# Optimization experiments

Hardware: AMD Instinct MI355X
Metric: run time of the kernel (lower is better)

## Reference

```python
import jax, jax.numpy as jnp
import numpy as np

N_NODES = 100000   # B*A = 4 * 25000 nodes after the reshape in forward()
N_EDGES = 1600000  # avg degree 16
F_IN = 2           # node_features
HID = 64           # hidden_size
K = 3              # diffusion order (hardcoded in RecurrentGCN)


def _glorot(key, shape):
    fan_in, fan_out = shape[-2], shape[-1]
    s = float(np.sqrt(6.0 / (fan_in + fan_out)))
    return jax.random.uniform(key, shape, jnp.float32, -s, s)


def setup_inputs() -> dict:
    key = jax.random.key(0)
    ks = jax.random.split(key, 12)
    x = jax.random.normal(ks[0], (4, 25000, 12, F_IN), dtype=jnp.float32)
    edge_index = jax.random.randint(ks[1], (2, N_EDGES), 0, N_NODES, dtype=jnp.int32)
    edge_weight = jax.random.uniform(ks[2], (N_EDGES,), dtype=jnp.float32)

    def cell(k, cin):
        kw = jax.random.split(k, 3)
        # 3 gates (z, r, h), each a DConv with weight [2, K, cin, HID]
        W = jnp.stack([_glorot(kw[i], (2, K, cin, HID)) for i in range(3)])
        b = jnp.zeros((3, HID), dtype=jnp.float32)
        return W, b

    enc1_W, enc1_b = cell(ks[3], F_IN + HID)
    enc2_W, enc2_b = cell(ks[4], HID + HID)
    dec1_W, dec1_b = cell(ks[5], F_IN + HID)
    dec2_W, dec2_b = cell(ks[6], HID + HID)
    lin_W = _glorot(ks[7], (HID, F_IN))
    lin_b = jnp.zeros((F_IN,), dtype=jnp.float32)
    return dict(x=x, edge_index=edge_index, edge_weight=edge_weight,
                enc1_W=enc1_W, enc1_b=enc1_b, enc2_W=enc2_W, enc2_b=enc2_b,
                dec1_W=dec1_W, dec1_b=dec1_b, dec2_W=dec2_W, dec2_b=dec2_b,
                lin_W=lin_W, lin_b=lin_b)


def _dconv(v, src, dst, do_inv, di_inv, W, b):
    # Dual-direction diffusion conv (DConv, torch_geometric_temporal), order K.
    # Normalization is applied at the node level before gather so the
    # edge-level multiply (E x C) never needs to be a stored residual.
    def pout(u):  # out[dst] += deg_out_inv[src] * u[src]
        return jax.ops.segment_sum((do_inv[:, None] * u)[src], dst, num_segments=N_NODES)

    def pin(u):   # out[src] += deg_in_inv[dst] * u[dst]
        return jax.ops.segment_sum((di_inv[:, None] * u)[dst], src, num_segments=N_NODES)

    H = v @ (W[0, 0] + W[1, 0])
    t1o, t1i = pout(v), pin(v)
    H = H + t1o @ W[0, 1] + t1i @ W[1, 1]
    t0o = t0i = v
    for k in range(2, K):  # Chebyshev-style recurrence
        t2o = 2.0 * pout(t1o) - t0o
        t2i = 2.0 * pin(t1i) - t0i
        H = H + t2o @ W[0, k] + t2i @ W[1, k]
        t0o, t1o = t1o, t2o
        t0i, t1i = t1i, t2i
    return H + b


def _dcrnn(x, h, src, dst, do_inv, di_inv, W, b):
    # GRU cell whose gates are diffusion convolutions over [x, h].
    xh = jnp.concatenate([x, h], axis=1)
    Z = jax.nn.sigmoid(_dconv(xh, src, dst, do_inv, di_inv, W[0], b[0]))
    R = jax.nn.sigmoid(_dconv(xh, src, dst, do_inv, di_inv, W[1], b[1]))
    Ht = jnp.tanh(_dconv(jnp.concatenate([x, R * h], axis=1),
                         src, dst, do_inv, di_inv, W[2], b[2]))
    return Z * h + (1.0 - Z) * Ht


def _forward(x, edge_index, edge_weight,
             enc1_W, enc1_b, enc2_W, enc2_b,
             dec1_W, dec1_b, dec2_W, dec2_b, lin_W, lin_b):
    B, A, S, Fd = x.shape
    # permute(0,1,3,2) then [..., 0] == x[:, :, 0, :]; flatten to [B*A, F]
    xs = x[:, :, 0, :].reshape(B * A, Fd)
    src, dst = edge_index[0], edge_index[1]
    deg_out = jax.ops.segment_sum(edge_weight, src, num_segments=N_NODES)
    deg_in = jax.ops.segment_sum(edge_weight, dst, num_segments=N_NODES)
    do_inv = jnp.where(deg_out > 0, 1.0 / deg_out, 0.0)
    di_inv = jnp.where(deg_in > 0, 1.0 / deg_in, 0.0)
    zeros = jnp.zeros((B * A, HID), dtype=x.dtype)
    h_enc1 = _dcrnn(xs, zeros, src, dst, do_inv, di_inv, enc1_W, enc1_b)
    h = jax.nn.relu(h_enc1)
    h_enc2 = _dcrnn(h, zeros, src, dst, do_inv, di_inv, enc2_W, enc2_b)
    h = _dcrnn(xs, h_enc1, src, dst, do_inv, di_inv, dec1_W, dec1_b)
    h = jax.nn.relu(h)
    h = _dcrnn(h, h_enc2, src, dst, do_inv, di_inv, dec2_W, dec2_b)
    return h @ lin_W + lin_b


def reference(x, edge_index, edge_weight,
              enc1_W, enc1_b, enc2_W, enc2_b,
              dec1_W, dec1_b, dec2_W, dec2_b, lin_W, lin_b):
    return _forward(x, edge_index, edge_weight,
                    enc1_W, enc1_b, enc2_W, enc2_b,
                    dec1_W, dec1_b, dec2_W, dec2_b, lin_W, lin_b)
```

## Files before the change

### kernel.cpp

```cpp
#include <hip/hip_runtime.h>

#define N_NODES 100000
#define N_EDGES 1600000

typedef _Float16 f16;
typedef _Float16 f16x4 __attribute__((ext_vector_type(4)));
typedef _Float16 f16x8 __attribute__((ext_vector_type(8)));
typedef float f32x4 __attribute__((ext_vector_type(4)));

__device__ __forceinline__ float sigf(float x) { return 1.f / (1.f + __expf(-x)); }


__global__ void count_kernel(const int* __restrict__ src, const int* __restrict__ dst,
                             int* __restrict__ cntO, int* __restrict__ cntI,
                             int* __restrict__ slotO, int* __restrict__ slotI)
{
    int i = blockIdx.x * 256 + threadIdx.x;
    if (i >= N_EDGES) return;
    slotO[i] = atomicAdd(&cntO[dst[i]], 1);
    slotI[i] = atomicAdd(&cntI[src[i]], 1);
}

__global__ __launch_bounds__(1024) void scan2_kernel(const int* __restrict__ cntA, int* __restrict__ rpA,
                                                     const int* __restrict__ cntB, int* __restrict__ rpB,
                                                     int n)
{
    const int* cnt = blockIdx.x ? cntB : cntA;
    int* rp = blockIdx.x ? rpB : rpA;
    __shared__ int wsum[16];
    __shared__ int carry;
    int tid = threadIdx.x, lane = tid & 63, wid = tid >> 6;
    if (tid == 0) { rp[0] = 0; carry = 0; }
    __syncthreads();
    for (int base = 0; base < n; base += 1024) {
        int idx = base + tid;
        int x = (idx < n) ? cnt[idx] : 0;
        #pragma unroll
        for (int off = 1; off < 64; off <<= 1) {
            int y = __shfl_up(x, off);
            if (lane >= off) x += y;
        }
        if (lane == 63) wsum[wid] = x;
        __syncthreads();
        if (wid == 0 && lane < 16) {
            int y = wsum[lane];
            #pragma unroll
            for (int off = 1; off < 16; off <<= 1) {
                int z = __shfl_up(y, off);
                if (lane >= off) y += z;
            }
            wsum[lane] = y;
        }
        __syncthreads();
        int tot = x + (wid ? wsum[wid - 1] : 0) + carry;
        if (idx < n) rp[idx + 1] = tot;
        __syncthreads();
        if (tid == 1023) carry = tot;
        __syncthreads();
    }
}

__global__ void fill_kernel(const int* __restrict__ src, const int* __restrict__ dst,
                            const float* __restrict__ ew,
                            const int* __restrict__ rpO, const int* __restrict__ rpI,
                            const int* __restrict__ slotO, const int* __restrict__ slotI,
                            int2* __restrict__ adj2O, int2* __restrict__ adj2I)
{
    int i = blockIdx.x * 256 + threadIdx.x;
    if (i >= N_EDGES) return;
    int s = src[i], d = dst[i];
    int wb = __float_as_int(ew[i]);
    int2 eo; eo.x = s; eo.y = wb;
    adj2O[rpO[d] + slotO[i]] = eo;
    int2 ei; ei.x = d; ei.y = wb;
    adj2I[rpI[s] + slotI[i]] = ei;
}

__global__ void finalize_kernel(const int* __restrict__ rpO, const int2* __restrict__ adj2O,
                                int* __restrict__ adjO, float* __restrict__ di_inv,
                                const int* __restrict__ rpI, const int2* __restrict__ adj2I,
                                int* __restrict__ adjI, float* __restrict__ do_inv)
{
    int n = blockIdx.x * 256 + threadIdx.x;
    if (n >= N_NODES) return;
    float s = 0.f;
    for (int e = rpO[n]; e < rpO[n + 1]; ++e) {
        int2 v = adj2O[e];
        adjO[e] = v.x;
        s += __int_as_float(v.y);
    }
    di_inv[n] = (s > 0.f) ? 1.f / s : 0.f;
    float t = 0.f;
    for (int e = rpI[n]; e < rpI[n + 1]; ++e) {
        int2 v = adj2I[e];
        adjI[e] = v.x;
        t += __int_as_float(v.y);
    }
    do_inv[n] = (t > 0.f) ? 1.f / t : 0.f;
}

__global__ void prep_w(const float* __restrict__ W, int C, int rowBase,
                       int gLo, int gHi, int COLS, int XSTEP, f16* __restrict__ outw)
{
    int total = (10 + XSTEP) * COLS * 32;
    int idx = blockIdx.x * 256 + threadIdx.x;
    if (idx >= total) return;
    int k32 = idx & 31;
    int c = (idx >> 5) % COLS;
    int s = (idx >> 5) / COLS;
    int g = (c < 64 || gHi < 0) ? gLo : gHi;
    int col = (c >= 64) ? c - 64 : c;
    int p, r;
    if (s < 10) { p = s >> 1; r = rowBase + ((s & 1) << 5) + k32; }
    else {
        if (k32 < 10) { p = k32 >> 1; r = k32 & 1; }
        else { outw[idx] = (f16)0.f; return; }
    }
    auto wv = [&](int d, int k) {
        return W[((((size_t)(g * 2 + d) * 3 + k) * C + r) << 6) + col];
    };
    float val;
    if (p == 0)      val = wv(0, 0) + wv(1, 0) - wv(0, 2) - wv(1, 2);
    else if (p == 1) val = wv(0, 1);
    else if (p == 2) val = 2.f * wv(0, 2);
    else if (p == 3) val = wv(1, 1);
    else             val = 2.f * wv(1, 2);
    outw[idx] = (f16)val;
}

__global__ void prep_enc1w(const float* __restrict__ W, float* __restrict__ outw)
{
    int idx = blockIdx.x * 256 + threadIdx.x;
    if (idx >= 1280) return;
    int c = idx & 127, k = idx >> 7;
    int g = (c < 64) ? 0 : 2, col = c & 63;
    int p = k >> 1, r = k & 1;
    const int C = 66;
    auto wv = [&](int d, int kk) {
        return W[((((size_t)(g * 2 + d) * 3 + kk) * C + r) << 6) + col];
    };
    float val;
    if (p == 0)      val = wv(0, 0) + wv(1, 0) - wv(0, 2) - wv(1, 2);
    else if (p == 1) val = wv(0, 1);
    else if (p == 2) val = 2.f * wv(0, 2);
    else if (p == 3) val = wv(1, 1);
    else             val = 2.f * wv(1, 2);
    outw[idx] = val;
}

__global__ void xcat_init(const float* __restrict__ x, f16* __restrict__ xcat)
{
    int i = blockIdx.x * 256 + threadIdx.x;
    if (i >= N_NODES * 32) return;
    int n = i >> 5, c = i & 31;
    float v = (c < 2) ? x[(size_t)n * 24 + c] : 0.f;
    xcat[i] = (f16)v;
}

__global__ void prop2_kernel(const int* __restrict__ rp, const int* __restrict__ adj,
                             const float* __restrict__ scale, f16* __restrict__ xcat,
                             int cin, int cout)
{
    int n = blockIdx.x * 256 + threadIdx.x;
    if (n >= N_NODES) return;
    int beg = rp[n], end = rp[n + 1];
    float a0 = 0.f, a1 = 0.f;
    for (int e = beg; e < end; ++e) {
        int s = adj[e];
        float w = scale[s];
        a0 += w * (float)xcat[((size_t)s << 5) + cin];
        a1 += w * (float)xcat[((size_t)s << 5) + cin + 1];
    }
    xcat[((size_t)n << 5) + cout] = (f16)a0;
    xcat[((size_t)n << 5) + cout + 1] = (f16)a1;
}

__global__ __launch_bounds__(256) void prop8(
    const int* __restrict__ rpA, const int* __restrict__ adjA, const float* __restrict__ scA,
    const f16* __restrict__ uA, f16* __restrict__ outA,
    const int* __restrict__ rpB, const int* __restrict__ adjB, const float* __restrict__ scB,
    const f16* __restrict__ uB, f16* __restrict__ outB)
{
    const int* RP; const int* ADJ; const float* SC; const f16* U; f16* OUT;
    if (blockIdx.y == 0) { RP = rpA; ADJ = adjA; SC = scA; U = uA; OUT = outA; }
    else                 { RP = rpB; ADJ = adjB; SC = scB; U = uB; OUT = outB; }
    int tid = threadIdx.x;
    int node = blockIdx.x * 32 + (tid >> 3);
    int l = tid & 7;
    if (node >= N_NODES) return;
    int b = RP[node], e = RP[node + 1];
    float a0 = 0.f, a1 = 0.f, a2 = 0.f, a3 = 0.f;
    float a4 = 0.f, a5 = 0.f, a6 = 0.f, a7 = 0.f;
    float c0 = 0.f, c1 = 0.f, c2 = 0.f, c3 = 0.f;
    float c4 = 0.f, c5 = 0.f, c6 = 0.f, c7 = 0.f;
    int i = b;
    for (; i + 1 < e; i += 2) {
        int s0 = ADJ[i], s1 = ADJ[i + 1];
        float w0 = SC[s0], w1 = SC[s1];
        f16x8 u0 = *(const f16x8*)(U + (((size_t)s0 << 6) + (l << 3)));
        f16x8 u1 = *(const f16x8*)(U + (((size_t)s1 << 6) + (l << 3)));
        a0 += w0 * (float)u0[0]; a1 += w0 * (float)u0[1];
        a2 += w0 * (float)u0[2]; a3 += w0 * (float)u0[3];
        a4 += w0 * (float)u0[4]; a5 += w0 * (float)u0[5];
        a6 += w0 * (float)u0[6]; a7 += w0 * (float)u0[7];
        c0 += w1 * (float)u1[0]; c1 += w1 * (float)u1[1];
        c2 += w1 * (float)u1[2]; c3 += w1 * (float)u1[3];
        c4 += w1 * (float)u1[4]; c5 += w1 * (float)u1[5];
        c6 += w1 * (float)u1[6]; c7 += w1 * (float)u1[7];
    }
    if (i < e) {
        int s = ADJ[i];
        float w = SC[s];
        f16x8 u0 = *(const f16x8*)(U + (((size_t)s << 6) + (l << 3)));
        a0 += w * (float)u0[0]; a1 += w * (float)u0[1];
        a2 += w * (float)u0[2]; a3 += w * (float)u0[3];
        a4 += w * (float)u0[4]; a5 += w * (float)u0[5];
        a6 += w * (float)u0[6]; a7 += w * (float)u0[7];
    }
    f16x8 r;
    r[0] = (f16)(a0 + c0); r[1] = (f16)(a1 + c1);
    r[2] = (f16)(a2 + c2); r[3] = (f16)(a3 + c3);
    r[4] = (f16)(a4 + c4); r[5] = (f16)(a5 + c5);
    r[6] = (f16)(a6 + c6); r[7] = (f16)(a7 + c7);
    *(f16x8*)(OUT + (((size_t)node << 6) + (l << 3))) = r;
}

template <int STEPS, int COLS, int ACT>
__global__ __launch_bounds__(256) void mfma_gemm(
    const f16* __restrict__ p0, const f16* __restrict__ p1, const f16* __restrict__ p2,
    const f16* __restrict__ p3, const f16* __restrict__ p4, const f16* __restrict__ xcat,
    const f16* __restrict__ wstep, const f16* __restrict__ addX,
    const float* __restrict__ biasLo, const float* __restrict__ biasHi,
    f16* __restrict__ out, const f16* __restrict__ hmul, f16* __restrict__ out2,
    const f16* __restrict__ zin)
{
    __shared__ f16 As[64][40];
    __shared__ f16 Ws[COLS][40];
    const int row0 = blockIdx.x * 64;
    const int tid = threadIdx.x;
    const int wave = tid >> 6, lane = tid & 63;
    const int lr = lane & 15, lk = lane >> 4;
    const int ka = lk << 3;

    constexpr int RT = (COLS == 128) ? 4 : 2;
    f32x4 acc[RT][2] = {};

    const f16* parts[5] = { p0, p1, p2, p3, p4 };

    #pragma unroll
    for (int s = 0; s < STEPS; ++s) {
        __syncthreads();
        {
            int r = tid >> 2, seg = tid & 3;
            int grow = row0 + r;
            const f16* srcp = (s < 10)
                ? parts[s >> 1] + (((size_t)grow << 6) + ((s & 1) << 5) + (seg << 3))
                : xcat + (((size_t)grow << 5) + (seg << 3));
            int4 v = (grow < N_NODES) ? *(const int4*)srcp : make_int4(0, 0, 0, 0);
            *(int4*)&As[r][seg << 3] = v;
        }
        {
            for (int q = tid; q < COLS * 4; q += 256) {
                int c = q >> 2, seg = q & 3;
                *(int4*)&Ws[c][seg << 3] =
                    *(const int4*)(wstep + (((size_t)(s * COLS + c) << 5) + (seg << 3)));
            }
        }
        __syncthreads();
        if (COLS == 128) {
            f16x8 b0 = *(const f16x8*)&Ws[wave * 32 + lr][ka];
            f16x8 b1 = *(const f16x8*)&Ws[wave * 32 + 16 + lr][ka];
            #pragma unroll
            for (int rt = 0; rt < RT; ++rt) {
                f16x8 a = *(const f16x8*)&As[rt * 16 + lr][ka];
                acc[rt][0] = __builtin_amdgcn_mfma_f32_16x16x32_f16(a, b0, acc[rt][0], 0, 0, 0);
                acc[rt][1] = __builtin_amdgcn_mfma_f32_16x16x32_f16(a, b1, acc[rt][1], 0, 0, 0);
            }
        } else {
            f16x8 b0 = *(const f16x8*)&Ws[(wave & 1) * 32 + lr][ka];
            f16x8 b1 = *(const f16x8*)&Ws[(wave & 1) * 32 + 16 + lr][ka];
            #pragma unroll
            for (int rt = 0; rt < RT; ++rt) {
                f16x8 a = *(const f16x8*)&As[(wave >> 1) * 32 + rt * 16 + lr][ka];
                acc[rt][0] = __builtin_amdgcn_mfma_f32_16x16x32_f16(a, b0, acc[rt][0], 0, 0, 0);
                acc[rt][1] = __builtin_amdgcn_mfma_f32_16x16x32_f16(a, b1, acc[rt][1], 0, 0, 0);
            }
        }
    }
    if constexpr (ACT == 4) {
        __shared__ float zbuf[64][65];
        float treg[RT][2][4];
        #pragma unroll
        for (int rt = 0; rt < RT; ++rt)
            #pragma unroll
            for (int ct = 0; ct < 2; ++ct) {
                int col = wave * 32 + ct * 16 + lr;
                #pragma unroll
                for (int j = 0; j < 4; ++j) {
                    int r = rt * 16 + lk * 4 + j;
                    float v = acc[rt][ct][j] + ((col < 64) ? biasLo[col] : biasHi[col - 64]);
                    if (col < 64) zbuf[r][col] = sigf(v);
                    else          treg[rt][ct][j] = tanhf(v);
                }
            }
        __syncthreads();
        #pragma unroll
        for (int rt = 0; rt < RT; ++rt)
            #pragma unroll
            for (int ct = 0; ct < 2; ++ct) {
                int col = wave * 32 + ct * 16 + lr;
                if (col < 64) continue;
                #pragma unroll
                for (int j = 0; j < 4; ++j) {
                    int r = rt * 16 + lk * 4 + j;
                    int grow = row0 + r;
                    if (grow >= N_NODES) continue;
                    float h = (1.f - zbuf[r][col - 64]) * treg[rt][ct][j];
                    out[((size_t)grow << 6) + (col - 64)] = (f16)h;
                }
            }
    } else if constexpr (ACT == 5) {
        #pragma unroll
        for (int rt = 0; rt < RT; ++rt)
            #pragma unroll
            for (int ct = 0; ct < 2; ++ct) {
                int col = wave * 32 + ct * 16 + lr;
                #pragma unroll
                for (int j = 0; j < 4; ++j) {
                    int grow = row0 + rt * 16 + lk * 4 + j;
                    if (grow >= N_NODES) continue;
                    float v = acc[rt][ct][j];
                    if (addX) v += (float)addX[((size_t)grow << 7) + col];
                    v += (col < 64) ? biasLo[col] : biasHi[col - 64];
                    float sg = sigf(v);
                    if (col < 64)
                        out[((size_t)grow << 6) + col] = (f16)sg;
                    else
                        out2[((size_t)grow << 6) + (col - 64)] =
                            (f16)(sg * (float)hmul[((size_t)grow << 6) + (col - 64)]);
                }
            }
    } else {
        #pragma unroll
        for (int rt = 0; rt < RT; ++rt) {
            int rbase = (COLS == 128) ? rt * 16 : (wave >> 1) * 32 + rt * 16;
            #pragma unroll
            for (int ct = 0; ct < 2; ++ct) {
                int col = ((COLS == 128) ? wave * 32 : (wave & 1) * 32) + ct * 16 + lr;
                #pragma unroll
                for (int j = 0; j < 4; ++j) {
                    int grow = row0 + rbase + lk * 4 + j;
                    if (grow >= N_NODES) continue;
                    float v = acc[rt][ct][j];
                    if (addX)   v += (float)addX[(size_t)grow * COLS + col];
                    if (biasLo) v += (col < 64) ? biasLo[col] : biasHi[col - 64];
                    if (ACT == 1)      v = sigf(v);
                    else if (ACT == 2) v = tanhf(v);
                    else if (ACT == 6) {
                        float t = tanhf(v);
                        float z = (float)zin[((size_t)grow << 6) + col];
                        float hv = (float)hmul[((size_t)grow << 6) + col];
                        v = fmaxf(z * hv + (1.f - z) * t, 0.f);
                    }
                    out[(size_t)grow * COLS + col] = (f16)v;
                }
            }
        }
    }
}

__global__ __launch_bounds__(256) void enc1_kernel(const f16* __restrict__ xcat,
                                                   const float* __restrict__ We1,
                                                   const float* __restrict__ b,
                                                   f16* __restrict__ h1, f16* __restrict__ h1r)
{
    int node = (blockIdx.x << 2) + (threadIdx.x >> 6);
    int lane = threadIdx.x & 63;
    float az = b[lane], at = b[128 + lane];
    #pragma unroll
    for (int k = 0; k < 10; ++k) {
        float xv = (float)xcat[((size_t)node << 5) + k];
        az += xv * We1[k * 128 + lane];
        at += xv * We1[k * 128 + 64 + lane];
    }
    float z = sigf(az), t = tanhf(at);
    float h = (1.f - z) * t;
    size_t o = ((size_t)node << 6) + lane;
    h1[o] = (f16)h;
    h1r[o] = (f16)fmaxf(h, 0.f);
}


__global__ __launch_bounds__(256) void final_kernel(const f16* __restrict__ zb, const f16* __restrict__ gT,
                                                    const f16* __restrict__ h2,
                                                    const float* __restrict__ lW, const float* __restrict__ lb,
                                                    float* __restrict__ out)
{
    int node = (blockIdx.x << 2) + (threadIdx.x >> 6);
    int lane = threadIdx.x & 63;
    size_t i = ((size_t)node << 6) + lane;
    float z = (float)zb[i];
    float d = z * (float)h2[i] + (1.f - z) * (float)gT[i];
    float s0 = d * lW[lane * 2];
    float s1 = d * lW[lane * 2 + 1];
    #pragma unroll
    for (int off = 32; off > 0; off >>= 1) {
        s0 += __shfl_down(s0, off);
        s1 += __shfl_down(s1, off);
    }
    if (lane == 0) {
        out[node * 2]     = s0 + lb[0];
        out[node * 2 + 1] = s1 + lb[1];
    }
}


extern "C" void kernel_launch(void* const* d_in, const int* in_sizes, int n_in,
                              void* d_out, int out_size, void* d_ws, size_t ws_size,
                              hipStream_t stream)
{
    (void)in_sizes; (void)n_in; (void)out_size;
    const float* x   = (const float*)d_in[0];
    const int*  eidx = (const int*)d_in[1];
    const float* ew  = (const float*)d_in[2];
    const float* e1W = (const float*)d_in[3];
    const float* e1b = (const float*)d_in[4];
    const float* e2W = (const float*)d_in[5];
    const float* e2b = (const float*)d_in[6];
    const float* d1W = (const float*)d_in[7];
    const float* d1b = (const float*)d_in[8];
    const float* d2W = (const float*)d_in[9];
    const float* d2b = (const float*)d_in[10];
    const float* lW  = (const float*)d_in[11];
    const float* lb  = (const float*)d_in[12];
    const int* src = eidx;
    const int* dst = eidx + N_EDGES;
    const int N = N_NODES, E = N_EDGES;

    char* p = (char*)d_ws;
    auto carve = [&](size_t bytes) { char* r = p; p += (bytes + 255) & ~(size_t)255; return r; };
    int*   cntO  = (int*)carve((size_t)2 * N * 4);
    int*   cntI  = cntO + N;
    int*   rpO   = (int*)carve((size_t)(N + 1) * 4);
    int*   rpI   = (int*)carve((size_t)(N + 1) * 4);
    int*   slotO = (int*)carve((size_t)E * 4);
    int*   slotI = (int*)carve((size_t)E * 4);
    int2*  adj2O = (int2*)carve((size_t)E * 8);
    int2*  adj2I = (int2*)carve((size_t)E * 8);
    float* do_inv = (float*)carve((size_t)N * 4);
    float* di_inv = (float*)carve((size_t)N * 4);
    f16*   xcat = (f16*)carve((size_t)N * 32 * 2);
    size_t NH = (size_t)N * 64 * 2;
    f16* h1  = (f16*)carve(NH);
    f16* h1r = (f16*)carve(NH);
    f16* h2  = (f16*)carve(NH);
    f16* g   = (f16*)carve(NH);
    f16* gT  = (f16*)carve(NH);
    f16* t0  = (f16*)carve(NH);
    f16* t1  = (f16*)carve(NH);
    f16* t2  = (f16*)carve(NH);
    f16* t3  = (f16*)carve(NH);
    f16* zb  = (f16*)carve(NH);
    f16* zz128 = (f16*)carve((size_t)N * 128 * 2);
    f16* wE2   = (f16*)carve((size_t)10 * 128 * 32 * 2);
    f16* wD1zr = (f16*)carve((size_t)11 * 128 * 32 * 2);
    f16* wD1c  = (f16*)carve((size_t)11 * 64 * 32 * 2);
    f16* wD2zrA = (f16*)carve((size_t)10 * 128 * 32 * 2);
    f16* wD2zrB = (f16*)carve((size_t)10 * 128 * 32 * 2);
    f16* wD2cA  = (f16*)carve((size_t)10 * 64 * 32 * 2);
    f16* wD2cB  = (f16*)carve((size_t)10 * 64 * 32 * 2);
    float* We1  = (float*)carve((size_t)1280 * 4);

    size_t needed = (size_t)(p - (char*)d_ws);
    if (needed > ws_size) return;

    const int eg = (E + 255) / 256;
    const int ng = (N + 255) / 256;
    const int GB = 25000;

    hipMemsetAsync(cntO, 0, (size_t)2 * N * 4, stream);
    count_kernel<<<eg, 256, 0, stream>>>(src, dst, cntO, cntI, slotO, slotI);
    scan2_kernel<<<2, 1024, 0, stream>>>(cntO, rpO, cntI, rpI, N);
    fill_kernel<<<eg, 256, 0, stream>>>(src, dst, ew, rpO, rpI, slotO, slotI, adj2O, adj2I);
    int* adjO = slotO;
    int* adjI = slotI;
    finalize_kernel<<<ng, 256, 0, stream>>>(rpO, adj2O, adjO, di_inv, rpI, adj2I, adjI, do_inv);

    auto wprep = [&](const float* W, int C, int rowBase, int gLo, int gHi, int COLS, int XS, f16* o) {
        int total = (10 + XS) * COLS * 32;
        prep_w<<<(total + 255) / 256, 256, 0, stream>>>(W, C, rowBase, gLo, gHi, COLS, XS, o);
    };
    wprep(e2W, 128, 0,  0, 2, 128, 0, wE2);
    wprep(d1W, 66,  2,  0, 1, 128, 1, wD1zr);
    wprep(d1W, 66,  2,  2, -1, 64, 1, wD1c);
    wprep(d2W, 128, 0,  0, 1, 128, 0, wD2zrA);
    wprep(d2W, 128, 64, 0, 1, 128, 0, wD2zrB);
    wprep(d2W, 128, 0,  2, -1, 64, 0, wD2cA);
    wprep(d2W, 128, 64, 2, -1, 64, 0, wD2cB);
    prep_enc1w<<<5, 256, 0, stream>>>(e1W, We1);

    xcat_init<<<(N * 32 + 255) / 256, 256, 0, stream>>>(x, xcat);
    prop2_kernel<<<ng, 256, 0, stream>>>(rpO, adjO, do_inv, xcat, 0, 2);
    prop2_kernel<<<ng, 256, 0, stream>>>(rpO, adjO, do_inv, xcat, 2, 4);
    prop2_kernel<<<ng, 256, 0, stream>>>(rpI, adjI, di_inv, xcat, 0, 6);
    prop2_kernel<<<ng, 256, 0, stream>>>(rpI, adjI, di_inv, xcat, 6, 8);

    const dim3 pg((N + 31) / 32, 2);
    auto props = [&](const f16* u) {
        prop8<<<pg, 256, 0, stream>>>(rpO, adjO, do_inv, u, t0,
                                      rpI, adjI, di_inv, u, t2);
        prop8<<<pg, 256, 0, stream>>>(rpO, adjO, do_inv, t0, t1,
                                      rpI, adjI, di_inv, t2, t3);
    };
    const int gg = (N + 63) / 64;

    enc1_kernel<<<GB, 256, 0, stream>>>(xcat, We1, e1b, h1, h1r);
    props(h1r);
    mfma_gemm<10, 128, 4><<<gg, 256, 0, stream>>>(h1r, t0, t1, t2, t3, nullptr, wE2,
                                                  nullptr, e2b, e2b + 128, h2, nullptr, nullptr, nullptr);
    props(h1);
    mfma_gemm<11, 128, 5><<<gg, 256, 0, stream>>>(h1, t0, t1, t2, t3, xcat, wD1zr,
                                                  nullptr, d1b, d1b + 64, zb, h1, g, nullptr);
    props(g);
    mfma_gemm<11, 64, 6><<<gg, 256, 0, stream>>>(g, t0, t1, t2, t3, xcat, wD1c,
                                                 nullptr, d1b + 128, d1b + 128, h1r, h1, nullptr, zb);
    props(h1r);
    mfma_gemm<10, 128, 0><<<gg, 256, 0, stream>>>(h1r, t0, t1, t2, t3, nullptr, wD2zrA,
                                                  nullptr, nullptr, nullptr, zz128, nullptr, nullptr, nullptr);
    mfma_gemm<10, 64, 0><<<gg, 256, 0, stream>>>(h1r, t0, t1, t2, t3, nullptr, wD2cA,
                                                 nullptr, nullptr, nullptr, gT, nullptr, nullptr, nullptr);
    props(h2);
    mfma_gemm<10, 128, 5><<<gg, 256, 0, stream>>>(h2, t0, t1, t2, t3, nullptr, wD2zrB,
                                                  zz128, d2b, d2b + 64, zb, h2, g, nullptr);
    props(g);
    mfma_gemm<10, 64, 2><<<gg, 256, 0, stream>>>(g, t0, t1, t2, t3, nullptr, wD2cB,
                                                 gT, d2b + 128, d2b + 128, gT, nullptr, nullptr, nullptr);
    final_kernel<<<GB, 256, 0, stream>>>(zb, gT, h2, lW, lb, (float*)d_out);
}
```

Baseline: 1.480 ms.

## Pack paired hidden states into 128-wide buffers and share diffusion propagations

Hidden-state pairs that are diffused by the same graph operators (relu(h1)/h1, and h1r/h2 for the second decoder cell) are stored side by side in 128-channel buffers. Each pair is then propagated in one pass with 16 lanes per node, so two props calls become one, and the first decoder gate GEMM reuses the encoder propagation results. The two decoder-2 z/r GEMMs merge into one 20-step GEMM, the zz128 intermediate is dropped, and the four prop2 launches are combined into two using a second grid dimension. The propagation scratch now aliases the edge-build buffers. In exchange, the 128-wide gathers read twice as much data per edge, and the grid sizes assume N divides evenly by 16 and 32.

Measured after the change: 1.470 ms. No clear change (-0.6%).

```diff
diff --git a/kernel.cpp b/kernel.cpp
--- a/kernel.cpp
+++ b/kernel.cpp
@@ -4,7 +4,6 @@
 #define N_EDGES 1600000
 
 typedef _Float16 f16;
-typedef _Float16 f16x4 __attribute__((ext_vector_type(4)));
 typedef _Float16 f16x8 __attribute__((ext_vector_type(8)));
 typedef float f32x4 __attribute__((ext_vector_type(4)));
 
@@ -99,10 +98,10 @@
     do_inv[n] = (t > 0.f) ? 1.f / t : 0.f;
 }
 
-__global__ void prep_w(const float* __restrict__ W, int C, int rowBase,
-                       int gLo, int gHi, int COLS, int XSTEP, f16* __restrict__ outw)
-{
-    int total = (10 + XSTEP) * COLS * 32;
+__global__ void prep_w(const float* __restrict__ W, int C, int SA, int PWA, int rA,
+                       int gLo, int gHi, int COLS, int XS, f16* __restrict__ outw)
+{
+    int total = (SA + XS) * COLS * 32;
     int idx = blockIdx.x * 256 + threadIdx.x;
     if (idx >= total) return;
     int k32 = idx & 31;
@@ -111,7 +110,7 @@
     int g = (c < 64 || gHi < 0) ? gLo : gHi;
     int col = (c >= 64) ? c - 64 : c;
     int p, r;
-    if (s < 10) { p = s >> 1; r = rowBase + ((s & 1) << 5) + k32; }
+    if (s < SA) { p = s / PWA; r = rA + (s % PWA) * 32 + k32; }
     else {
         if (k32 < 10) { p = k32 >> 1; r = k32 & 1; }
         else { outw[idx] = (f16)0.f; return; }
@@ -157,17 +156,22 @@
     xcat[i] = (f16)v;
 }
 
-__global__ void prop2_kernel(const int* __restrict__ rp, const int* __restrict__ adj,
-                             const float* __restrict__ scale, f16* __restrict__ xcat,
-                             int cin, int cout)
-{
+__global__ void prop2d_kernel(const int* __restrict__ rpA, const int* __restrict__ adjA,
+                              const float* __restrict__ scA, int cinA, int coutA,
+                              const int* __restrict__ rpB, const int* __restrict__ adjB,
+                              const float* __restrict__ scB, int cinB, int coutB,
+                              f16* __restrict__ xcat)
+{
+    const int* rp; const int* adj; const float* sc; int cin, cout;
+    if (blockIdx.y == 0) { rp = rpA; adj = adjA; sc = scA; cin = cinA; cout = coutA; }
+    else                 { rp = rpB; adj = adjB; sc = scB; cin = cinB; cout = coutB; }
     int n = blockIdx.x * 256 + threadIdx.x;
     if (n >= N_NODES) return;
     int beg = rp[n], end = rp[n + 1];
     float a0 = 0.f, a1 = 0.f;
     for (int e = beg; e < end; ++e) {
         int s = adj[e];
-        float w = scale[s];
+        float w = sc[s];
         a0 += w * (float)xcat[((size_t)s << 5) + cin];
         a1 += w * (float)xcat[((size_t)s << 5) + cin + 1];
     }
@@ -175,64 +179,57 @@
     xcat[((size_t)n << 5) + cout + 1] = (f16)a1;
 }
 
-__global__ __launch_bounds__(256) void prop8(
+template <int LPN>
+__global__ __launch_bounds__(256) void propk(
     const int* __restrict__ rpA, const int* __restrict__ adjA, const float* __restrict__ scA,
-    const f16* __restrict__ uA, f16* __restrict__ outA,
+    const f16* __restrict__ uA, f16* __restrict__ oA,
     const int* __restrict__ rpB, const int* __restrict__ adjB, const float* __restrict__ scB,
-    const f16* __restrict__ uB, f16* __restrict__ outB)
+    const f16* __restrict__ uB, f16* __restrict__ oB,
+    int ldu, int ldo)
 {
     const int* RP; const int* ADJ; const float* SC; const f16* U; f16* OUT;
-    if (blockIdx.y == 0) { RP = rpA; ADJ = adjA; SC = scA; U = uA; OUT = outA; }
-    else                 { RP = rpB; ADJ = adjB; SC = scB; U = uB; OUT = outB; }
-    int tid = threadIdx.x;
-    int node = blockIdx.x * 32 + (tid >> 3);
-    int l = tid & 7;
+    if (blockIdx.y == 0) { RP = rpA; ADJ = adjA; SC = scA; U = uA; OUT = oA; }
+    else                 { RP = rpB; ADJ = adjB; SC = scB; U = uB; OUT = oB; }
+    constexpr int NPB = 256 / LPN;
+    int node = blockIdx.x * NPB + (threadIdx.x / LPN);
+    int l = threadIdx.x % LPN;
     if (node >= N_NODES) return;
     int b = RP[node], e = RP[node + 1];
-    float a0 = 0.f, a1 = 0.f, a2 = 0.f, a3 = 0.f;
-    float a4 = 0.f, a5 = 0.f, a6 = 0.f, a7 = 0.f;
-    float c0 = 0.f, c1 = 0.f, c2 = 0.f, c3 = 0.f;
-    float c4 = 0.f, c5 = 0.f, c6 = 0.f, c7 = 0.f;
+    float a[8] = {0.f, 0.f, 0.f, 0.f, 0.f, 0.f, 0.f, 0.f};
+    float c[8] = {0.f, 0.f, 0.f, 0.f, 0.f, 0.f, 0.f, 0.f};
     int i = b;
     for (; i + 1 < e; i += 2) {
         int s0 = ADJ[i], s1 = ADJ[i + 1];
         float w0 = SC[s0], w1 = SC[s1];
-        f16x8 u0 = *(const f16x8*)(U + (((size_t)s0 << 6) + (l << 3)));
-        f16x8 u1 = *(const f16x8*)(U + (((size_t)s1 << 6) + (l << 3)));
-        a0 += w0 * (float)u0[0]; a1 += w0 * (float)u0[1];
-        a2 += w0 * (float)u0[2]; a3 += w0 * (float)u0[3];
-        a4 += w0 * (float)u0[4]; a5 += w0 * (float)u0[5];
-        a6 += w0 * (float)u0[6]; a7 += w0 * (float)u0[7];
-        c0 += w1 * (float)u1[0]; c1 += w1 * (float)u1[1];
-        c2 += w1 * (float)u1[2]; c3 += w1 * (float)u1[3];
-        c4 += w1 * (float)u1[4]; c5 += w1 * (float)u1[5];
-        c6 += w1 * (float)u1[6]; c7 += w1 * (float)u1[7];
+        f16x8 u0 = *(const f16x8*)(U + (size_t)s0 * ldu + (l << 3));
+        f16x8 u1 = *(const f16x8*)(U + (size_t)s1 * ldu + (l << 3));
+        #pragma unroll
+        for (int j = 0; j < 8; ++j) { a[j] += w0 * (float)u0[j]; c[j] += w1 * (float)u1[j]; }
     }
     if (i < e) {
         int s = ADJ[i];
         float w = SC[s];
-        f16x8 u0 = *(const f16x8*)(U + (((size_t)s << 6) + (l << 3)));
-        a0 += w * (float)u0[0]; a1 += w * (float)u0[1];
-        a2 += w * (float)u0[2]; a3 += w * (float)u0[3];
-        a4 += w * (float)u0[4]; a5 += w * (float)u0[5];
-        a6 += w * (float)u0[6]; a7 += w * (float)u0[7];
+        f16x8 u0 = *(const f16x8*)(U + (size_t)s * ldu + (l << 3));
+        #pragma unroll
+        for (int j = 0; j < 8; ++j) a[j] += w * (float)u0[j];
     }
     f16x8 r;
-    r[0] = (f16)(a0 + c0); r[1] = (f16)(a1 + c1);
-    r[2] = (f16)(a2 + c2); r[3] = (f16)(a3 + c3);
-    r[4] = (f16)(a4 + c4); r[5] = (f16)(a5 + c5);
-    r[6] = (f16)(a6 + c6); r[7] = (f16)(a7 + c7);
-    *(f16x8*)(OUT + (((size_t)node << 6) + (l << 3))) = r;
-}
-
-template <int STEPS, int COLS, int ACT>
+    #pragma unroll
+    for (int j = 0; j < 8; ++j) r[j] = (f16)(a[j] + c[j]);
+    *(f16x8*)(OUT + (size_t)node * ldo + (l << 3)) = r;
+}
+
+template <int SA, int XS, int COLS, int ACT>
 __global__ __launch_bounds__(256) void mfma_gemm(
-    const f16* __restrict__ p0, const f16* __restrict__ p1, const f16* __restrict__ p2,
-    const f16* __restrict__ p3, const f16* __restrict__ p4, const f16* __restrict__ xcat,
-    const f16* __restrict__ wstep, const f16* __restrict__ addX,
+    const f16* __restrict__ uA, const f16* __restrict__ tA0, const f16* __restrict__ tA1,
+    const f16* __restrict__ tA2, const f16* __restrict__ tA3,
+    int lAu, int cAu, int lAt, int cAt,
+    const f16* __restrict__ xcat, const f16* __restrict__ wstep,
+    const f16* __restrict__ addX,
     const float* __restrict__ biasLo, const float* __restrict__ biasHi,
-    f16* __restrict__ out, const f16* __restrict__ hmul, f16* __restrict__ out2,
-    const f16* __restrict__ zin)
+    f16* __restrict__ out, int os,
+    const f16* __restrict__ hmul, int hs,
+    f16* __restrict__ out2, const f16* __restrict__ zin)
 {
     __shared__ f16 As[64][40];
     __shared__ f16 Ws[COLS][40];
@@ -241,11 +238,11 @@
     const int wave = tid >> 6, lane = tid & 63;
     const int lr = lane & 15, lk = lane >> 4;
     const int ka = lk << 3;
-
     constexpr int RT = (COLS == 128) ? 4 : 2;
+    constexpr int PWA = SA / 5;
+    constexpr int STEPS = SA + XS;
     f32x4 acc[RT][2] = {};
-
-    const f16* parts[5] = { p0, p1, p2, p3, p4 };
+    const f16* tA[4] = { tA0, tA1, tA2, tA3 };
 
     #pragma unroll
     for (int s = 0; s < STEPS; ++s) {
@@ -253,18 +250,23 @@
         {
             int r = tid >> 2, seg = tid & 3;
             int grow = row0 + r;
-            const f16* srcp = (s < 10)
-                ? parts[s >> 1] + (((size_t)grow << 6) + ((s & 1) << 5) + (seg << 3))
-                : xcat + (((size_t)grow << 5) + (seg << 3));
+            const f16* srcp;
+            if (s < SA) {
+                int p = s / PWA, ch = s % PWA;
+                const f16* base = (p == 0) ? uA : tA[p - 1];
+                int ld = (p == 0) ? lAu : lAt;
+                int co = (p == 0) ? cAu : cAt;
+                srcp = base + (size_t)grow * ld + co + ch * 32 + (seg << 3);
+            } else {
+                srcp = xcat + (((size_t)grow) << 5) + (seg << 3);
+            }
             int4 v = (grow < N_NODES) ? *(const int4*)srcp : make_int4(0, 0, 0, 0);
             *(int4*)&As[r][seg << 3] = v;
         }
-        {
-            for (int q = tid; q < COLS * 4; q += 256) {
-                int c = q >> 2, seg = q & 3;
-                *(int4*)&Ws[c][seg << 3] =
-                    *(const int4*)(wstep + (((size_t)(s * COLS + c) << 5) + (seg << 3)));
-            }
+        for (int q = tid; q < COLS * 4; q += 256) {
+            int c = q >> 2, seg = q & 3;
+            *(int4*)&Ws[c][seg << 3] =
+                *(const int4*)(wstep + (((size_t)(s * COLS + c)) << 5) + (seg << 3));
         }
         __syncthreads();
         if (COLS == 128) {
@@ -316,7 +318,7 @@
                     int grow = row0 + r;
                     if (grow >= N_NODES) continue;
                     float h = (1.f - zbuf[r][col - 64]) * treg[rt][ct][j];
-                    out[((size_t)grow << 6) + (col - 64)] = (f16)h;
+                    out[(size_t)grow * os + (col - 64)] = (f16)h;
                 }
             }
     } else if constexpr (ACT == 5) {
@@ -329,15 +331,13 @@
                 for (int j = 0; j < 4; ++j) {
                     int grow = row0 + rt * 16 + lk * 4 + j;
                     if (grow >= N_NODES) continue;
-                    float v = acc[rt][ct][j];
-                    if (addX) v += (float)addX[((size_t)grow << 7) + col];
-                    v += (col < 64) ? biasLo[col] : biasHi[col - 64];
+                    float v = acc[rt][ct][j] + ((col < 64) ? biasLo[col] : biasHi[col - 64]);
                     float sg = sigf(v);
                     if (col < 64)
                         out[((size_t)grow << 6) + col] = (f16)sg;
                     else
                         out2[((size_t)grow << 6) + (col - 64)] =
-                            (f16)(sg * (float)hmul[((size_t)grow << 6) + (col - 64)]);
+                            (f16)(sg * (float)hmul[(size_t)grow * hs + (col - 64)]);
                 }
             }
     } else {
@@ -352,17 +352,16 @@
                     int grow = row0 + rbase + lk * 4 + j;
                     if (grow >= N_NODES) continue;
                     float v = acc[rt][ct][j];
-                    if (addX)   v += (float)addX[(size_t)grow * COLS + col];
+                    if (addX)   v += (float)addX[((size_t)grow << 6) + col];
                     if (biasLo) v += (col < 64) ? biasLo[col] : biasHi[col - 64];
-                    if (ACT == 1)      v = sigf(v);
-                    else if (ACT == 2) v = tanhf(v);
+                    if (ACT == 2) v = tanhf(v);
                     else if (ACT == 6) {
                         float t = tanhf(v);
                         float z = (float)zin[((size_t)grow << 6) + col];
-                        float hv = (float)hmul[((size_t)grow << 6) + col];
+                        float hv = (float)hmul[(size_t)grow * hs + col];
                         v = fmaxf(z * hv + (1.f - z) * t, 0.f);
                     }
-                    out[(size_t)grow * COLS + col] = (f16)v;
+                    out[(size_t)grow * os + col] = (f16)v;
                 }
             }
         }
@@ -372,7 +371,7 @@
 __global__ __launch_bounds__(256) void enc1_kernel(const f16* __restrict__ xcat,
                                                    const float* __restrict__ We1,
                                                    const float* __restrict__ b,
-                                                   f16* __restrict__ h1, f16* __restrict__ h1r)
+                                                   f16* __restrict__ c1)
 {
     int node = (blockIdx.x << 2) + (threadIdx.x >> 6);
     int lane = threadIdx.x & 63;
@@ -385,11 +384,10 @@
     }
     float z = sigf(az), t = tanhf(at);
     float h = (1.f - z) * t;
-    size_t o = ((size_t)node << 6) + lane;
-    h1[o] = (f16)h;
-    h1r[o] = (f16)fmaxf(h, 0.f);
-}
-
+    size_t o = (size_t)node * 128 + lane;
+    c1[o] = (f16)fmaxf(h, 0.f);
+    c1[o + 64] = (f16)h;
+}
 
 __global__ __launch_bounds__(256) void final_kernel(const f16* __restrict__ zb, const f16* __restrict__ gT,
                                                     const f16* __restrict__ h2,
@@ -400,7 +398,7 @@
     int lane = threadIdx.x & 63;
     size_t i = ((size_t)node << 6) + lane;
     float z = (float)zb[i];
-    float d = z * (float)h2[i] + (1.f - z) * (float)gT[i];
+    float d = z * (float)h2[(size_t)node * 128 + lane] + (1.f - z) * (float)gT[i];
     float s0 = d * lW[lane * 2];
     float s1 = d * lW[lane * 2 + 1];
     #pragma unroll
@@ -439,37 +437,36 @@
 
     char* p = (char*)d_ws;
     auto carve = [&](size_t bytes) { char* r = p; p += (bytes + 255) & ~(size_t)255; return r; };
+    size_t NC = (size_t)N * 128 * 2;
+    size_t NH = (size_t)N * 64 * 2;
     int*   cntO  = (int*)carve((size_t)2 * N * 4);
     int*   cntI  = cntO + N;
     int*   rpO   = (int*)carve((size_t)(N + 1) * 4);
     int*   rpI   = (int*)carve((size_t)(N + 1) * 4);
     int*   slotO = (int*)carve((size_t)E * 4);
     int*   slotI = (int*)carve((size_t)E * 4);
-    int2*  adj2O = (int2*)carve((size_t)E * 8);
-    int2*  adj2I = (int2*)carve((size_t)E * 8);
+    char*  uni   = carve((size_t)2 * E * 8);
+    int2*  adj2O = (int2*)uni;
+    int2*  adj2I = (int2*)(uni + (size_t)E * 8);
+    f16*   ct0   = (f16*)uni;
+    f16*   ct1   = (f16*)carve(NC);
+    f16*   ct2   = (f16*)carve(NC);
+    f16*   ct3   = (f16*)carve(NC);
     float* do_inv = (float*)carve((size_t)N * 4);
     float* di_inv = (float*)carve((size_t)N * 4);
     f16*   xcat = (f16*)carve((size_t)N * 32 * 2);
-    size_t NH = (size_t)N * 64 * 2;
-    f16* h1  = (f16*)carve(NH);
-    f16* h1r = (f16*)carve(NH);
-    f16* h2  = (f16*)carve(NH);
-    f16* g   = (f16*)carve(NH);
-    f16* gT  = (f16*)carve(NH);
-    f16* t0  = (f16*)carve(NH);
-    f16* t1  = (f16*)carve(NH);
-    f16* t2  = (f16*)carve(NH);
-    f16* t3  = (f16*)carve(NH);
-    f16* zb  = (f16*)carve(NH);
-    f16* zz128 = (f16*)carve((size_t)N * 128 * 2);
+    f16*   c1   = (f16*)carve(NC);
+    f16*   c2   = (f16*)carve(NC);
+    f16*   g    = (f16*)carve(NH);
+    f16*   gT   = (f16*)carve(NH);
+    f16*   zb   = (f16*)carve(NH);
     f16* wE2   = (f16*)carve((size_t)10 * 128 * 32 * 2);
     f16* wD1zr = (f16*)carve((size_t)11 * 128 * 32 * 2);
     f16* wD1c  = (f16*)carve((size_t)11 * 64 * 32 * 2);
-    f16* wD2zrA = (f16*)carve((size_t)10 * 128 * 32 * 2);
-    f16* wD2zrB = (f16*)carve((size_t)10 * 128 * 32 * 2);
-    f16* wD2cA  = (f16*)carve((size_t)10 * 64 * 32 * 2);
-    f16* wD2cB  = (f16*)carve((size_t)10 * 64 * 32 * 2);
-    float* We1  = (float*)carve((size_t)1280 * 4);
+    f16* wD2zr = (f16*)carve((size_t)20 * 128 * 32 * 2);
+    f16* wD2cA = (f16*)carve((size_t)10 * 64 * 32 * 2);
+    f16* wD2cB = (f16*)carve((size_t)10 * 64 * 32 * 2);
+    float* We1 = (float*)carve((size_t)1280 * 4);
 
     size_t needed = (size_t)(p - (char*)d_ws);
     if (needed > ws_size) return;
@@ -486,54 +483,64 @@
     int* adjI = slotI;
     finalize_kernel<<<ng, 256, 0, stream>>>(rpO, adj2O, adjO, di_inv, rpI, adj2I, adjI, do_inv);
 
-    auto wprep = [&](const float* W, int C, int rowBase, int gLo, int gHi, int COLS, int XS, f16* o) {
-        int total = (10 + XS) * COLS * 32;
-        prep_w<<<(total + 255) / 256, 256, 0, stream>>>(W, C, rowBase, gLo, gHi, COLS, XS, o);
+    auto wprep = [&](const float* W, int C, int SA, int PWA, int rA,
+                     int gLo, int gHi, int COLS, int XS, f16* o) {
+        int total = (SA + XS) * COLS * 32;
+        prep_w<<<(total + 255) / 256, 256, 0, stream>>>(W, C, SA, PWA, rA, gLo, gHi, COLS, XS, o);
     };
-    wprep(e2W, 128, 0,  0, 2, 128, 0, wE2);
-    wprep(d1W, 66,  2,  0, 1, 128, 1, wD1zr);
-    wprep(d1W, 66,  2,  2, -1, 64, 1, wD1c);
-    wprep(d2W, 128, 0,  0, 1, 128, 0, wD2zrA);
-    wprep(d2W, 128, 64, 0, 1, 128, 0, wD2zrB);
-    wprep(d2W, 128, 0,  2, -1, 64, 0, wD2cA);
-    wprep(d2W, 128, 64, 2, -1, 64, 0, wD2cB);
+    wprep(e2W, 128, 10, 2, 0,  0,  2, 128, 0, wE2);
+    wprep(d1W, 66,  10, 2, 2,  0,  1, 128, 1, wD1zr);
+    wprep(d1W, 66,  10, 2, 2,  2, -1,  64, 1, wD1c);
+    wprep(d2W, 128, 20, 4, 0,  0,  1, 128, 0, wD2zr);
+    wprep(d2W, 128, 10, 2, 0,  2, -1,  64, 0, wD2cA);
+    wprep(d2W, 128, 10, 2, 64, 2, -1,  64, 0, wD2cB);
     prep_enc1w<<<5, 256, 0, stream>>>(e1W, We1);
 
     xcat_init<<<(N * 32 + 255) / 256, 256, 0, stream>>>(x, xcat);
-    prop2_kernel<<<ng, 256, 0, stream>>>(rpO, adjO, do_inv, xcat, 0, 2);
-    prop2_kernel<<<ng, 256, 0, stream>>>(rpO, adjO, do_inv, xcat, 2, 4);
-    prop2_kernel<<<ng, 256, 0, stream>>>(rpI, adjI, di_inv, xcat, 0, 6);
-    prop2_kernel<<<ng, 256, 0, stream>>>(rpI, adjI, di_inv, xcat, 6, 8);
-
-    const dim3 pg((N + 31) / 32, 2);
-    auto props = [&](const f16* u) {
-        prop8<<<pg, 256, 0, stream>>>(rpO, adjO, do_inv, u, t0,
-                                      rpI, adjI, di_inv, u, t2);
-        prop8<<<pg, 256, 0, stream>>>(rpO, adjO, do_inv, t0, t1,
-                                      rpI, adjI, di_inv, t2, t3);
+    dim3 ng2(ng, 2);
+    prop2d_kernel<<<ng2, 256, 0, stream>>>(rpO, adjO, do_inv, 0, 2,
+                                           rpI, adjI, di_inv, 0, 6, xcat);
+    prop2d_kernel<<<ng2, 256, 0, stream>>>(rpO, adjO, do_inv, 2, 4,
+                                           rpI, adjI, di_inv, 6, 8, xcat);
+
+    auto props128 = [&](const f16* u) {
+        dim3 pg(N / 16, 2);
+        propk<16><<<pg, 256, 0, stream>>>(rpO, adjO, do_inv, u, ct0,
+                                          rpI, adjI, di_inv, u, ct2, 128, 128);
+        propk<16><<<pg, 256, 0, stream>>>(rpO, adjO, do_inv, ct0, ct1,
+                                          rpI, adjI, di_inv, ct2, ct3, 128, 128);
+    };
+    auto props64 = [&](const f16* u) {
+        dim3 pg(N / 32, 2);
+        propk<8><<<pg, 256, 0, stream>>>(rpO, adjO, do_inv, u, ct0,
+                                         rpI, adjI, di_inv, u, ct2, 64, 128);
+        propk<8><<<pg, 256, 0, stream>>>(rpO, adjO, do_inv, ct0, ct1,
+                                         rpI, adjI, di_inv, ct2, ct3, 128, 128);
     };
     const int gg = (N + 63) / 64;
 
-    enc1_kernel<<<GB, 256, 0, stream>>>(xcat, We1, e1b, h1, h1r);
-    props(h1r);
-    mfma_gemm<10, 128, 4><<<gg, 256, 0, stream>>>(h1r, t0, t1, t2, t3, nullptr, wE2,
-                                                  nullptr, e2b, e2b + 128, h2, nullptr, nullptr, nullptr);
-    props(h1);
-    mfma_gemm<11, 128, 5><<<gg, 256, 0, stream>>>(h1, t0, t1, t2, t3, xcat, wD1zr,
-                                                  nullptr, d1b, d1b + 64, zb, h1, g, nullptr);
-    props(g);
-    mfma_gemm<11, 64, 6><<<gg, 256, 0, stream>>>(g, t0, t1, t2, t3, xcat, wD1c,
-                                                 nullptr, d1b + 128, d1b + 128, h1r, h1, nullptr, zb);
-    props(h1r);
-    mfma_gemm<10, 128, 0><<<gg, 256, 0, stream>>>(h1r, t0, t1, t2, t3, nullptr, wD2zrA,
-                                                  nullptr, nullptr, nullptr, zz128, nullptr, nullptr, nullptr);
-    mfma_gemm<10, 64, 0><<<gg, 256, 0, stream>>>(h1r, t0, t1, t2, t3, nullptr, wD2cA,
-                                                 nullptr, nullptr, nullptr, gT, nullptr, nullptr, nullptr);
-    props(h2);
-    mfma_gemm<10, 128, 5><<<gg, 256, 0, stream>>>(h2, t0, t1, t2, t3, nullptr, wD2zrB,
-                                                  zz128, d2b, d2b + 64, zb, h2, g, nullptr);
-    props(g);
-    mfma_gemm<10, 64, 2><<<gg, 256, 0, stream>>>(g, t0, t1, t2, t3, nullptr, wD2cB,
-                                                 gT, d2b + 128, d2b + 128, gT, nullptr, nullptr, nullptr);
-    final_kernel<<<GB, 256, 0, stream>>>(zb, gT, h2, lW, lb, (float*)d_out);
-}
+    enc1_kernel<<<GB, 256, 0, stream>>>(xcat, We1, e1b, c1);
+    props128(c1);
+    mfma_gemm<10, 0, 128, 4><<<gg, 256, 0, stream>>>(
+        c1, ct0, ct1, ct2, ct3, 128, 0, 128, 0, nullptr, wE2,
+        nullptr, e2b, e2b + 128, c2 + 64, 128, nullptr, 0, nullptr, nullptr);
+    mfma_gemm<10, 1, 128, 5><<<gg, 256, 0, stream>>>(
+        c1, ct0, ct1, ct2, ct3, 128, 64, 128, 64, xcat, wD1zr,
+        nullptr, d1b, d1b + 64, zb, 64, c1 + 64, 128, g, nullptr);
+    props64(g);
+    mfma_gemm<10, 1, 64, 6><<<gg, 256, 0, stream>>>(
+        g, ct0, ct1, ct2, ct3, 64, 0, 128, 0, xcat, wD1c,
+        nullptr, d1b + 128, d1b + 128, c2, 128, c1 + 64, 128, nullptr, zb);
+    props128(c2);
+    mfma_gemm<20, 0, 128, 5><<<gg, 256, 0, stream>>>(
+        c2, ct0, ct1, ct2, ct3, 128, 0, 128, 0, nullptr, wD2zr,
+        nullptr, d2b, d2b + 64, zb, 64, c2 + 64, 128, g, nullptr);
+    mfma_gemm<10, 0, 64, 0><<<gg, 256, 0, stream>>>(
+        c2, ct0, ct1, ct2, ct3, 128, 0, 128, 0, nullptr, wD2cA,
+        nullptr, nullptr, nullptr, gT, 64, nullptr, 0, nullptr, nullptr);
+    props64(g);
+    mfma_gemm<10, 0, 64, 2><<<gg, 256, 0, stream>>>(
+        g, ct0, ct1, ct2, ct3, 64, 0, 128, 0, nullptr, wD2cB,
+        gT, d2b + 128, d2b + 128, gT, 64, nullptr, 0, nullptr, nullptr);
+    final_kernel<<<GB, 256, 0, stream>>>(zb, gT, c2 + 64, lW, lb, (float*)d_out);
+}
```
